# Kernel tuning notes

Measured on AMD Instinct MI355X. Metric: run time of the kernel, lower is better.

Reference implementation:

```python
import jax, jax.numpy as jnp
import numpy as np

NEG_INF = -2.0**32 + 1.0  # matches torch paddings value


def prelu(x, a):
    return jnp.where(x >= 0, x, a * x)


def setup_inputs() -> dict:
    key = jax.random.key(0)
    ks = jax.random.split(key, 12)
    B, L, D, A = 2048, 200, 128, 64
    return {
        "query": jax.random.normal(ks[0], (B, D), jnp.float32),
        "keys": jax.random.normal(ks[1], (B, L, D), jnp.float32),
        "keys_length": jax.random.randint(ks[2], (B,), 0, L, jnp.int64 if jax.config.jax_enable_x64 else jnp.int32),
        "W1": jax.random.normal(ks[3], (4 * D, A), jnp.float32) * (1.0 / np.sqrt(4 * D)),
        "b1": jax.random.normal(ks[4], (A,), jnp.float32) * 0.01,
        "a1": jnp.full((1,), 0.25, jnp.float32),  # PReLU default init
        "W2": jax.random.normal(ks[5], (A, A), jnp.float32) * (1.0 / np.sqrt(A)),
        "b2": jax.random.normal(ks[6], (A,), jnp.float32) * 0.01,
        "a2": jnp.full((1,), 0.25, jnp.float32),
        "W3": jax.random.normal(ks[7], (A, 1), jnp.float32) * (1.0 / np.sqrt(A)),
        "b3": jax.random.normal(ks[8], (1,), jnp.float32) * 0.01,
    }


def reference(query, keys, keys_length, W1, b1, a1, W2, b2, a2, W3, b3):
    B, L, D = keys.shape
    q = jnp.broadcast_to(query[:, None, :], (B, L, D))
    # concat features: [q, k, q-k, q*k] -> (B, L, 4D)
    q_k = jnp.concatenate([q, keys, q - keys, q * keys], axis=-1)
    h = prelu(jnp.einsum("blf,fa->bla", q_k, W1) + b1, a1)
    h = prelu(jnp.einsum("bla,ac->blc", h, W2) + b2, a2)
    scores = (jnp.einsum("bla,ao->blo", h, W3) + b3)[..., 0]  # (B, L)
    mask = jnp.arange(L)[None, :] < keys_length[:, None]
    scores = jnp.where(mask, scores, NEG_INF)
    att = jax.nn.softmax(scores, axis=1)
    out = jnp.einsum("bl,bld->bd", att, keys)  # bmm(att[:,None,:], keys)
    return out, att
```

## Files before the change

kernel.cpp:

```cpp
#include <hip/hip_runtime.h>
#include <math.h>

typedef __attribute__((ext_vector_type(8))) _Float16 half8;
typedef __attribute__((ext_vector_type(4))) float float4_t;

#define NB 2048
#define LL 200
#define DD 128
#define AA 64
#define NEG_INF_F -4294967295.0f

#define WQ_STRIDE 136

#define WS_WBC_H  0
#define WS_W1D_H  8704
#define WS_W2T_H  17408
#define WS_QA_OFF 43008

__global__ __launch_bounds__(256)
void din_prep(const float* __restrict__ query,
              const float* __restrict__ W1,
              const float* __restrict__ b1,
              const float* __restrict__ W2,
              _Float16* __restrict__ ws16,
              float* __restrict__ qa)
{
    const int tid = threadIdx.x;
    const int blk = blockIdx.x;

    if (blk < 128) {
        __shared__ float sW1s[DD * AA];
        __shared__ float sq[16 * DD];
        const int b0 = blk * 16;
        for (int i = tid; i < DD * AA; i += 256)
            sW1s[i] = W1[i] + W1[2 * DD * AA + i];
        for (int i = tid; i < 16 * DD; i += 256)
            sq[i] = query[(size_t)b0 * DD + i];
        __syncthreads();
        const int lane = tid & 63, bb = tid >> 6;
        for (int g = 0; g < 4; ++g) {
            const int bi = bb * 4 + g;
            float acc = b1[lane];
            #pragma unroll 8
            for (int d = 0; d < DD; ++d)
                acc += sq[bi * DD + d] * sW1s[d * AA + lane];
            qa[(size_t)(b0 + bi) * AA + lane] = acc;
        }
    } else if (blk == 128) {
        for (int i = tid; i < 64 * 17; i += 256) {
            const int a = i / 17, c = i - a * 17;
            half8 hb, hd;
            if (c == 16) {
                #pragma unroll
                for (int j = 0; j < 8; ++j) { hb[j] = (_Float16)0.f; hd[j] = (_Float16)0.f; }
            } else {
                const int d0 = c * 8;
                #pragma unroll
                for (int j = 0; j < 8; ++j) {
                    const int d = d0 + j;
                    hb[j] = (_Float16)(W1[(DD + d) * AA + a] - W1[(2 * DD + d) * AA + a]);
                    hd[j] = (_Float16)(W1[(3 * DD + d) * AA + a]);
                }
            }
            *(half8*)&ws16[WS_WBC_H + a * WQ_STRIDE + c * 8] = hb;
            *(half8*)&ws16[WS_W1D_H + a * WQ_STRIDE + c * 8] = hd;
        }
    } else {
        _Float16* w2t = ws16 + WS_W2T_H;
        const int c = tid >> 2, j0 = (tid & 3) * 16;
        for (int ch = 0; ch < 2; ++ch) {
            half8 v;
            #pragma unroll
            for (int j = 0; j < 8; ++j)
                v[j] = (_Float16)W2[(j0 + ch * 8 + j) * AA + c];
            *(half8*)&w2t[c * AA + j0 + ch * 8] = v;
        }
    }
}

__global__ __launch_bounds__(512, 4)
void din_main(const float* __restrict__ keys,
              const int*   __restrict__ keys_length,
              const float* __restrict__ a1p,
              const float* __restrict__ b2,
              const float* __restrict__ a2p,
              const float* __restrict__ W3,
              const _Float16* __restrict__ ws16,
              const float* __restrict__ qa,
              const float* __restrict__ query,
              float* __restrict__ out,
              float* __restrict__ att)
{
    __shared__ __align__(16) _Float16 sKeys[LL * DD];
    __shared__ __align__(16) _Float16 sWq[AA * WQ_STRIDE];
    __shared__ __align__(16) _Float16 sH1[4 * 16 * 72];
    __shared__ float sQ[136];
    __shared__ float sS[224];
    __shared__ float sRed[16];

    const int tid  = threadIdx.x;
    const int lane = tid & 63, wv = tid >> 6;
    const int col  = lane & 15, quad = lane >> 4;
    const int b    = blockIdx.x;
    const int len  = keys_length[b];
    const float pa1 = a1p[0], pa2 = a2p[0];
    const int Lcap = (len == 0) ? LL : len;

    if (tid < 136) sQ[tid] = (tid < 128) ? query[(size_t)b * DD + tid] : 0.f;
    for (int i = tid; i < 224; i += 512) sS[i] = NEG_INF_F;
    __syncthreads();

    for (int ci = tid; ci < 64 * 17; ci += 512) {
        const int c = ci % 17;
        const int d0 = c * 8;
        const half8 hb = *(const half8*)&ws16[WS_WBC_H + ci * 8];
        const half8 hd = *(const half8*)&ws16[WS_W1D_H + ci * 8];
        half8 r;
        #pragma unroll
        for (int j = 0; j < 8; ++j)
            r[j] = (_Float16)((float)hb[j] + sQ[d0 + j] * (float)hd[j]);
        *(half8*)&sWq[ci * 8] = r;
    }
    for (int i = tid; i < Lcap * 16; i += 512) {
        const int l = i >> 4, c8 = i & 15;
        const float* kp = keys + ((size_t)b * LL + l) * DD + c8 * 8;
        const float4 v0 = *(const float4*)kp;
        const float4 v1 = *(const float4*)(kp + 4);
        half8 h;
        h[0] = (_Float16)v0.x; h[1] = (_Float16)v0.y; h[2] = (_Float16)v0.z; h[3] = (_Float16)v0.w;
        h[4] = (_Float16)v1.x; h[5] = (_Float16)v1.y; h[6] = (_Float16)v1.z; h[7] = (_Float16)v1.w;
        *(half8*)&sKeys[l * DD + ((c8 ^ (l & 7)) << 3)] = h;
    }
    __syncthreads();

    if (wv < 4) {
        const _Float16* w2t = ws16 + WS_W2T_H;
        half8 w2f[2][4];
        #pragma unroll
        for (int ks = 0; ks < 2; ++ks)
            #pragma unroll
            for (int n = 0; n < 4; ++n)
                w2f[ks][n] = *(const half8*)&w2t[(n * 16 + col) * AA + ks * 32 + quad * 8];
        float qareg[4], b2reg[4], w3reg[4];
        #pragma unroll
        for (int n = 0; n < 4; ++n) {
            qareg[n] = qa[(size_t)b * AA + n * 16 + col];
            b2reg[n] = b2[n * 16 + col];
            w3reg[n] = W3[n * 16 + col];
        }

        const int ntiles = (len + 15) >> 4;
        _Float16* const myH = &sH1[wv * 16 * 72];

        for (int t = wv; t < ntiles; t += 4) {
            const int l0 = t * 16;
            const int lr = (l0 + col < LL) ? (l0 + col) : (LL - 1);

            float4_t C[4] = {{0,0,0,0},{0,0,0,0},{0,0,0,0},{0,0,0,0}};
            #pragma unroll
            for (int ks = 0; ks < 4; ++ks) {
                const int swz = ((ks * 4 + quad) ^ (lr & 7)) << 3;
                const half8 af = *(const half8*)&sKeys[lr * DD + swz];
                const int ko = ks * 32 + quad * 8;
                #pragma unroll
                for (int n = 0; n < 4; ++n) {
                    const half8 bf = *(const half8*)&sWq[(n * 16 + col) * WQ_STRIDE + ko];
                    C[n] = __builtin_amdgcn_mfma_f32_16x16x32_f16(af, bf, C[n], 0, 0, 0);
                }
            }
            #pragma unroll
            for (int n = 0; n < 4; ++n)
                #pragma unroll
                for (int r = 0; r < 4; ++r) {
                    float v = C[n][r] + qareg[n];
                    v = v >= 0.f ? v : pa1 * v;
                    myH[(quad * 4 + r) * 72 + n * 16 + col] = (_Float16)v;
                }
            float4_t D[4] = {{0,0,0,0},{0,0,0,0},{0,0,0,0},{0,0,0,0}};
            #pragma unroll
            for (int ks = 0; ks < 2; ++ks) {
                const half8 af = *(const half8*)&myH[col * 72 + ks * 32 + quad * 8];
                #pragma unroll
                for (int n = 0; n < 4; ++n)
                    D[n] = __builtin_amdgcn_mfma_f32_16x16x32_f16(af, w2f[ks][n], D[n], 0, 0, 0);
            }
            float pr[4] = {0.f, 0.f, 0.f, 0.f};
            #pragma unroll
            for (int n = 0; n < 4; ++n)
                #pragma unroll
                for (int r = 0; r < 4; ++r) {
                    float v = D[n][r] + b2reg[n];
                    v = v >= 0.f ? v : pa2 * v;
                    pr[r] += v * w3reg[n];
                }
            #pragma unroll
            for (int r = 0; r < 4; ++r) {
                float pv = pr[r];
                pv += __shfl_xor(pv, 1);
                pv += __shfl_xor(pv, 2);
                pv += __shfl_xor(pv, 4);
                pv += __shfl_xor(pv, 8);
                const int l = l0 + quad * 4 + r;
                if (col == 0 && l < len) sS[l] = pv;
            }
        }
    }

    __syncthreads();
    float m = (tid < LL) ? sS[tid] : -INFINITY;
    #pragma unroll
    for (int o = 1; o < 64; o <<= 1) m = fmaxf(m, __shfl_xor(m, o));
    if (lane == 0) sRed[wv] = m;
    __syncthreads();
    float M = sRed[0];
    #pragma unroll
    for (int i = 1; i < 8; ++i) M = fmaxf(M, sRed[i]);
    float e = (tid < LL) ? expf(sS[tid] - M) : 0.f;
    float s = e;
    #pragma unroll
    for (int o = 1; o < 64; o <<= 1) s += __shfl_xor(s, o);
    if (lane == 0) sRed[8 + wv] = s;
    __syncthreads();
    float S = sRed[8];
    #pragma unroll
    for (int i = 9; i < 16; ++i) S += sRed[i];
    const float inv = 1.f / S;
    if (tid < LL) {
        const float v = e * inv;
        sS[tid] = v;
        att[(size_t)b * LL + tid] = v;
    }
    __syncthreads();

    {
        const int c8 = tid & 15, ph = tid >> 4;
        float acc[8];
        #pragma unroll
        for (int j = 0; j < 8; ++j) acc[j] = 0.f;
        for (int l = ph; l < Lcap; l += 32) {
            const float w = sS[l];
            const half8 kv = *(const half8*)&sKeys[l * DD + ((c8 ^ (l & 7)) << 3)];
            #pragma unroll
            for (int j = 0; j < 8; ++j) acc[j] += w * (float)kv[j];
        }
        float* const scratch = (float*)sWq;
        #pragma unroll
        for (int j = 0; j < 8; ++j) scratch[tid * 8 + j] = acc[j];
        __syncthreads();
        if (tid < DD) {
            const int c8o = tid >> 3, j = tid & 7;
            float r = 0.f;
            #pragma unroll
            for (int p = 0; p < 32; ++p) r += scratch[(p * 16 + c8o) * 8 + j];
            out[(size_t)b * DD + tid] = r;
        }
    }
}

extern "C" void kernel_launch(void* const* d_in, const int* in_sizes, int n_in,
                              void* d_out, int out_size, void* d_ws, size_t ws_size,
                              hipStream_t stream) {
    (void)in_sizes; (void)n_in; (void)ws_size; (void)out_size;
    const float* query = (const float*)d_in[0];
    const float* keys  = (const float*)d_in[1];
    const int*   klen  = (const int*)d_in[2];
    const float* W1    = (const float*)d_in[3];
    const float* b1    = (const float*)d_in[4];
    const float* a1    = (const float*)d_in[5];
    const float* W2    = (const float*)d_in[6];
    const float* b2    = (const float*)d_in[7];
    const float* a2    = (const float*)d_in[8];
    const float* W3    = (const float*)d_in[9];

    _Float16* ws16 = (_Float16*)d_ws;
    float*    qawk = (float*)((char*)d_ws + WS_QA_OFF);

    float* out = (float*)d_out;
    float* att = out + (size_t)NB * DD;

    hipLaunchKernelGGL(din_prep, dim3(130), dim3(256), 0, stream,
                       query, W1, b1, W2, ws16, qawk);
    hipLaunchKernelGGL(din_main, dim3(NB), dim3(512), 0, stream,
                       keys, klen, a1, b2, a2, W3, ws16, qawk, query, out, att);
}
```

Baseline: 326.1 us.

## Process four batches per block with double-buffered key prefetch

Each block now handles four consecutive batch rows instead of one. The keys for the next row are loaded into registers while the current row's MLP and softmax run, then written into a second LDS buffer. The per-block weight fragments are loaded once and reused across rows, and all eight waves now share the MLP tile work instead of four. The doubled key buffer roughly doubles LDS use and the register prefetch raises register pressure, so occupancy likely drops to one block per CU and load balance across the smaller grid may suffer.

```diff
diff --git a/kernel.cpp b/kernel.cpp
--- a/kernel.cpp
+++ b/kernel.cpp
@@ -8,6 +8,8 @@
 #define LL 200
 #define DD 128
 #define AA 64
+#define BPB 4
+#define NTHR 512
 #define NEG_INF_F -4294967295.0f
 
 #define WQ_STRIDE 136
@@ -78,7 +80,7 @@
     }
 }
 
-__global__ __launch_bounds__(512, 4)
+__global__ __launch_bounds__(NTHR, 2)
 void din_main(const float* __restrict__ keys,
               const int*   __restrict__ keys_length,
               const float* __restrict__ a1p,
@@ -91,68 +93,123 @@
               float* __restrict__ out,
               float* __restrict__ att)
 {
-    __shared__ __align__(16) _Float16 sKeys[LL * DD];
+    __shared__ __align__(16) _Float16 sKeys[2][LL * DD];
     __shared__ __align__(16) _Float16 sWq[AA * WQ_STRIDE];
-    __shared__ __align__(16) _Float16 sH1[4 * 16 * 72];
-    __shared__ float sQ[136];
+    __shared__ __align__(16) _Float16 sH1[8 * 16 * 72];
+    __shared__ float sQ[2][136];
     __shared__ float sS[224];
     __shared__ float sRed[16];
 
     const int tid  = threadIdx.x;
     const int lane = tid & 63, wv = tid >> 6;
     const int col  = lane & 15, quad = lane >> 4;
-    const int b    = blockIdx.x;
-    const int len  = keys_length[b];
+    const int b0   = blockIdx.x * BPB;
     const float pa1 = a1p[0], pa2 = a2p[0];
-    const int Lcap = (len == 0) ? LL : len;
-
-    if (tid < 136) sQ[tid] = (tid < 128) ? query[(size_t)b * DD + tid] : 0.f;
-    for (int i = tid; i < 224; i += 512) sS[i] = NEG_INF_F;
+
+    const int4 len4 = *(const int4*)&keys_length[b0];
+    const int lens[4] = {len4.x, len4.y, len4.z, len4.w};
+
+    half8 hbR[3], hdR[3];
+    #pragma unroll
+    for (int k = 0; k < 3; ++k) {
+        const int ci = tid + k * NTHR;
+        if (ci < 64 * 17) {
+            hbR[k] = *(const half8*)&ws16[WS_WBC_H + ci * 8];
+            hdR[k] = *(const half8*)&ws16[WS_W1D_H + ci * 8];
+        }
+    }
+    const _Float16* w2t = ws16 + WS_W2T_H;
+    half8 w2f[2][4];
+    #pragma unroll
+    for (int ks = 0; ks < 2; ++ks)
+        #pragma unroll
+        for (int n = 0; n < 4; ++n)
+            w2f[ks][n] = *(const half8*)&w2t[(n * 16 + col) * AA + ks * 32 + quad * 8];
+    float b2reg[4], w3reg[4], qaC[4];
+    #pragma unroll
+    for (int n = 0; n < 4; ++n) {
+        b2reg[n] = b2[n * 16 + col];
+        w3reg[n] = W3[n * 16 + col];
+        qaC[n]   = qa[(size_t)b0 * AA + n * 16 + col];
+    }
+
+    float qcur = 0.f;
+    if (tid < DD) qcur = query[(size_t)b0 * DD + tid];
+    if (tid >= DD && tid < 136) { sQ[0][tid] = 0.f; sQ[1][tid] = 0.f; }
+    {
+        const int len0  = lens[0];
+        const int Lcap0 = len0 ? len0 : LL;
+        const float* kbase = keys + (size_t)b0 * LL * DD;
+        #pragma unroll
+        for (int it = 0; it < 7; ++it) {
+            const int i = tid + it * NTHR;
+            if (i < Lcap0 * 16) {
+                const int l = i >> 4, c8 = i & 15;
+                const float* kp = kbase + l * DD + c8 * 8;
+                const float4 v0 = *(const float4*)kp;
+                const float4 v1 = *(const float4*)(kp + 4);
+                half8 h;
+                h[0] = (_Float16)v0.x; h[1] = (_Float16)v0.y;
+                h[2] = (_Float16)v0.z; h[3] = (_Float16)v0.w;
+                h[4] = (_Float16)v1.x; h[5] = (_Float16)v1.y;
+                h[6] = (_Float16)v1.z; h[7] = (_Float16)v1.w;
+                *(half8*)&sKeys[0][l * DD + ((c8 ^ (l & 7)) << 3)] = h;
+            }
+        }
+    }
+    if (tid < DD) sQ[0][tid] = qcur;
+    for (int i = tid; i < 224; i += NTHR) sS[i] = NEG_INF_F;
     __syncthreads();
-
-    for (int ci = tid; ci < 64 * 17; ci += 512) {
-        const int c = ci % 17;
-        const int d0 = c * 8;
-        const half8 hb = *(const half8*)&ws16[WS_WBC_H + ci * 8];
-        const half8 hd = *(const half8*)&ws16[WS_W1D_H + ci * 8];
-        half8 r;
-        #pragma unroll
-        for (int j = 0; j < 8; ++j)
-            r[j] = (_Float16)((float)hb[j] + sQ[d0 + j] * (float)hd[j]);
-        *(half8*)&sWq[ci * 8] = r;
-    }
-    for (int i = tid; i < Lcap * 16; i += 512) {
-        const int l = i >> 4, c8 = i & 15;
-        const float* kp = keys + ((size_t)b * LL + l) * DD + c8 * 8;
-        const float4 v0 = *(const float4*)kp;
-        const float4 v1 = *(const float4*)(kp + 4);
-        half8 h;
-        h[0] = (_Float16)v0.x; h[1] = (_Float16)v0.y; h[2] = (_Float16)v0.z; h[3] = (_Float16)v0.w;
-        h[4] = (_Float16)v1.x; h[5] = (_Float16)v1.y; h[6] = (_Float16)v1.z; h[7] = (_Float16)v1.w;
-        *(half8*)&sKeys[l * DD + ((c8 ^ (l & 7)) << 3)] = h;
+    #pragma unroll
+    for (int k = 0; k < 3; ++k) {
+        const int ci = tid + k * NTHR;
+        if (ci < 64 * 17) {
+            const int c = ci % 17, d0 = c * 8;
+            half8 r;
+            #pragma unroll
+            for (int j = 0; j < 8; ++j)
+                r[j] = (_Float16)((float)hbR[k][j] + sQ[0][d0 + j] * (float)hdR[k][j]);
+            *(half8*)&sWq[ci * 8] = r;
+        }
     }
     __syncthreads();
 
-    if (wv < 4) {
-        const _Float16* w2t = ws16 + WS_W2T_H;
-        half8 w2f[2][4];
-        #pragma unroll
-        for (int ks = 0; ks < 2; ++ks)
+    float4 kr[7][2];
+    float qnext = 0.f;
+    float qaN[4] = {0.f, 0.f, 0.f, 0.f};
+    int cur = 0;
+
+    for (int bi = 0; bi < BPB; ++bi) {
+        const int b      = b0 + bi;
+        const int len    = lens[bi];
+        const int Lcap   = len ? len : LL;
+        const int ntiles = (len + 15) >> 4;
+        const int nxt    = cur ^ 1;
+        const bool pf    = (bi + 1 < BPB);
+
+        int LcapN = 0;
+        if (pf) {
+            const int lenN = lens[bi + 1];
+            LcapN = lenN ? lenN : LL;
+            const float* kbase = keys + (size_t)(b + 1) * LL * DD;
+            #pragma unroll
+            for (int it = 0; it < 7; ++it) {
+                const int i = tid + it * NTHR;
+                if (i < LcapN * 16) {
+                    const int l = i >> 4, c8 = i & 15;
+                    const float* kp = kbase + l * DD + c8 * 8;
+                    kr[it][0] = *(const float4*)kp;
+                    kr[it][1] = *(const float4*)(kp + 4);
+                }
+            }
+            if (tid < DD) qnext = query[(size_t)(b + 1) * DD + tid];
             #pragma unroll
             for (int n = 0; n < 4; ++n)
-                w2f[ks][n] = *(const half8*)&w2t[(n * 16 + col) * AA + ks * 32 + quad * 8];
-        float qareg[4], b2reg[4], w3reg[4];
-        #pragma unroll
-        for (int n = 0; n < 4; ++n) {
-            qareg[n] = qa[(size_t)b * AA + n * 16 + col];
-            b2reg[n] = b2[n * 16 + col];
-            w3reg[n] = W3[n * 16 + col];
-        }
-
-        const int ntiles = (len + 15) >> 4;
+                qaN[n] = qa[(size_t)(b + 1) * AA + n * 16 + col];
+        }
+
         _Float16* const myH = &sH1[wv * 16 * 72];
-
-        for (int t = wv; t < ntiles; t += 4) {
+        for (int t = wv; t < ntiles; t += 8) {
             const int l0 = t * 16;
             const int lr = (l0 + col < LL) ? (l0 + col) : (LL - 1);
 
@@ -160,7 +217,7 @@
             #pragma unroll
             for (int ks = 0; ks < 4; ++ks) {
                 const int swz = ((ks * 4 + quad) ^ (lr & 7)) << 3;
-                const half8 af = *(const half8*)&sKeys[lr * DD + swz];
+                const half8 af = *(const half8*)&sKeys[cur][lr * DD + swz];
                 const int ko = ks * 32 + quad * 8;
                 #pragma unroll
                 for (int n = 0; n < 4; ++n) {
@@ -172,7 +229,7 @@
             for (int n = 0; n < 4; ++n)
                 #pragma unroll
                 for (int r = 0; r < 4; ++r) {
-                    float v = C[n][r] + qareg[n];
+                    float v = C[n][r] + qaC[n];
                     v = v >= 0.f ? v : pa1 * v;
                     myH[(quad * 4 + r) * 72 + n * 16 + col] = (_Float16)v;
                 }
@@ -204,56 +261,96 @@
                 if (col == 0 && l < len) sS[l] = pv;
             }
         }
-    }
-
-    __syncthreads();
-    float m = (tid < LL) ? sS[tid] : -INFINITY;
-    #pragma unroll
-    for (int o = 1; o < 64; o <<= 1) m = fmaxf(m, __shfl_xor(m, o));
-    if (lane == 0) sRed[wv] = m;
-    __syncthreads();
-    float M = sRed[0];
-    #pragma unroll
-    for (int i = 1; i < 8; ++i) M = fmaxf(M, sRed[i]);
-    float e = (tid < LL) ? expf(sS[tid] - M) : 0.f;
-    float s = e;
-    #pragma unroll
-    for (int o = 1; o < 64; o <<= 1) s += __shfl_xor(s, o);
-    if (lane == 0) sRed[8 + wv] = s;
-    __syncthreads();
-    float S = sRed[8];
-    #pragma unroll
-    for (int i = 9; i < 16; ++i) S += sRed[i];
-    const float inv = 1.f / S;
-    if (tid < LL) {
-        const float v = e * inv;
-        sS[tid] = v;
-        att[(size_t)b * LL + tid] = v;
-    }
-    __syncthreads();
-
-    {
-        const int c8 = tid & 15, ph = tid >> 4;
-        float acc[8];
-        #pragma unroll
-        for (int j = 0; j < 8; ++j) acc[j] = 0.f;
-        for (int l = ph; l < Lcap; l += 32) {
-            const float w = sS[l];
-            const half8 kv = *(const half8*)&sKeys[l * DD + ((c8 ^ (l & 7)) << 3)];
-            #pragma unroll
-            for (int j = 0; j < 8; ++j) acc[j] += w * (float)kv[j];
-        }
-        float* const scratch = (float*)sWq;
-        #pragma unroll
-        for (int j = 0; j < 8; ++j) scratch[tid * 8 + j] = acc[j];
-        __syncthreads();
-        if (tid < DD) {
-            const int c8o = tid >> 3, j = tid & 7;
-            float r = 0.f;
-            #pragma unroll
-            for (int p = 0; p < 32; ++p) r += scratch[(p * 16 + c8o) * 8 + j];
-            out[(size_t)b * DD + tid] = r;
-        }
+        __syncthreads();
+
+        float m = (tid < LL) ? sS[tid] : -INFINITY;
+        #pragma unroll
+        for (int o = 1; o < 64; o <<= 1) m = fmaxf(m, __shfl_xor(m, o));
+        if (lane == 0) sRed[wv] = m;
+        __syncthreads();
+        float M = sRed[0];
+        #pragma unroll
+        for (int i = 1; i < 8; ++i) M = fmaxf(M, sRed[i]);
+        float e = (tid < LL) ? expf(sS[tid] - M) : 0.f;
+        float s = e;
+        #pragma unroll
+        for (int o = 1; o < 64; o <<= 1) s += __shfl_xor(s, o);
+        if (lane == 0) sRed[8 + wv] = s;
+        __syncthreads();
+        float S = sRed[8];
+        #pragma unroll
+        for (int i = 9; i < 16; ++i) S += sRed[i];
+        const float inv = 1.f / S;
+        if (tid < LL) {
+            const float v = e * inv;
+            sS[tid] = v;
+            att[(size_t)b * LL + tid] = v;
+        }
+        __syncthreads();
+
+        if (pf && tid < DD) sQ[nxt][tid] = qnext;
+        {
+            const int c8 = tid & 15, ph = tid >> 4;
+            float acc[8];
+            #pragma unroll
+            for (int j = 0; j < 8; ++j) acc[j] = 0.f;
+            for (int l = ph; l < Lcap; l += 32) {
+                const float w = sS[l];
+                const half8 kv = *(const half8*)&sKeys[cur][l * DD + ((c8 ^ (l & 7)) << 3)];
+                #pragma unroll
+                for (int j = 0; j < 8; ++j) acc[j] += w * (float)kv[j];
+            }
+            float* const scratch = (float*)sH1;
+            #pragma unroll
+            for (int j = 0; j < 8; ++j) scratch[tid * 8 + j] = acc[j];
+        }
+        if (pf) {
+            #pragma unroll
+            for (int it = 0; it < 7; ++it) {
+                const int i = tid + it * NTHR;
+                if (i < LcapN * 16) {
+                    const int l = i >> 4, c8 = i & 15;
+                    const float4 v0 = kr[it][0], v1 = kr[it][1];
+                    half8 h;
+                    h[0] = (_Float16)v0.x; h[1] = (_Float16)v0.y;
+                    h[2] = (_Float16)v0.z; h[3] = (_Float16)v0.w;
+                    h[4] = (_Float16)v1.x; h[5] = (_Float16)v1.y;
+                    h[6] = (_Float16)v1.z; h[7] = (_Float16)v1.w;
+                    *(half8*)&sKeys[nxt][l * DD + ((c8 ^ (l & 7)) << 3)] = h;
+                }
+            }
+        }
+        __syncthreads();
+
+        {
+            const float* scratch = (const float*)sH1;
+            if (tid < DD) {
+                const int c8o = tid >> 3, j = tid & 7;
+                float r = 0.f;
+                #pragma unroll
+                for (int p = 0; p < 32; ++p) r += scratch[(p * 16 + c8o) * 8 + j];
+                out[(size_t)b * DD + tid] = r;
+            }
+        }
+        if (pf) {
+            #pragma unroll
+            for (int k = 0; k < 3; ++k) {
+                const int ci = tid + k * NTHR;
+                if (ci < 64 * 17) {
+                    const int c = ci % 17, d0 = c * 8;
+                    half8 r;
+                    #pragma unroll
+                    for (int j = 0; j < 8; ++j)
+                        r[j] = (_Float16)((float)hbR[k][j] + sQ[nxt][d0 + j] * (float)hdR[k][j]);
+                    *(half8*)&sWq[ci * 8] = r;
+                }
+            }
+            #pragma unroll
+            for (int n = 0; n < 4; ++n) qaC[n] = qaN[n];
+        }
+        for (int i = tid; i < 224; i += NTHR) sS[i] = NEG_INF_F;
+        __syncthreads();
+        cur = nxt;
     }
 }
 
@@ -280,6 +377,6 @@
 
     hipLaunchKernelGGL(din_prep, dim3(130), dim3(256), 0, stream,
                        query, W1, b1, W2, ws16, qawk);
-    hipLaunchKernelGGL(din_main, dim3(NB), dim3(512), 0, stream,
+    hipLaunchKernelGGL(din_main, dim3(NB / BPB), dim3(NTHR), 0, stream,
                        keys, klen, a1, b2, a2, W3, ws16, qawk, query, out, att);
 }
```

Result: slower. 365.0 us (+12.0%).
